# Kernel tuning notes

Hardware: AMD Instinct MI355X
Metric: run time of the kernel (lower is better)

## Reference

```python
import jax, jax.numpy as jnp
import numpy as np

D_MODEL = 1024
D_INDEX = 32
NUM_HEADS = 4
SEQ_LEN = 4096
BATCH = 2


def setup_inputs() -> dict:
    key = jax.random.key(0)
    ks = jax.random.split(key, 7)
    s = 1.0 / np.sqrt(D_MODEL)
    x = jax.random.normal(ks[0], (SEQ_LEN, BATCH, D_MODEL), dtype=jnp.float32)
    Wq = jax.random.uniform(ks[1], (D_MODEL, NUM_HEADS * D_INDEX), jnp.float32, -s, s)
    bq = jax.random.uniform(ks[2], (NUM_HEADS * D_INDEX,), jnp.float32, -s, s)
    Wk = jax.random.uniform(ks[3], (D_MODEL, D_INDEX), jnp.float32, -s, s)
    bk = jax.random.uniform(ks[4], (D_INDEX,), jnp.float32, -s, s)
    Ww = jax.random.uniform(ks[5], (D_MODEL, NUM_HEADS), jnp.float32, -s, s)
    bw = jax.random.uniform(ks[6], (NUM_HEADS,), jnp.float32, -s, s)
    return {"x": x, "Wq": Wq, "bq": bq, "Wk": Wk, "bk": bk, "Ww": Ww, "bw": bw}


def reference(x, Wq, bq, Wk, bk, Ww, bw):
    # x: [T, B, D] -> batch-first [B, T, D]
    xb = jnp.transpose(x, (1, 0, 2))
    B, T, _ = xb.shape
    q = (xb @ Wq + bq).reshape(B, T, NUM_HEADS, D_INDEX)  # [B,T,H,d]
    k = xb @ Wk + bk                                       # [B,T,d] (keys over s)
    w = xb @ Ww + bw                                       # [B,T,H]
    dot = jnp.einsum('bthd,bsd->btsh', q, k)               # [B,T,S,H]
    activated = jax.nn.relu(dot)
    # sum over heads weighted by w[b,t,h]
    index_scores = jnp.einsum('btsh,bth->bts', activated, w)
    return index_scores
```

## Files before the change

kernel.cpp:

```cpp
#include <hip/hip_runtime.h>

#define T_SEQ 4096
#define NBATCH 2
#define DM 1024
#define DI 32
#define NH 4
#define NCOLS 164
#define NCOLS_PAD 192
#define KC 64
#define BSTRIDE 72

typedef __attribute__((ext_vector_type(8))) short bf16x8;
typedef __attribute__((ext_vector_type(4))) float f32x4;

__device__ __forceinline__ unsigned short f2bf(float f) {
    unsigned int u = __builtin_bit_cast(unsigned int, f);
    u += 0x7FFFu + ((u >> 16) & 1u);
    return (unsigned short)(u >> 16);
}

__global__ __launch_bounds__(256) void prep_kernel(
    const float* __restrict__ Wq, const float* __restrict__ bq,
    const float* __restrict__ Wk, const float* __restrict__ bk,
    const float* __restrict__ Ww, const float* __restrict__ bw,
    unsigned short* __restrict__ WT, float* __restrict__ bias) {
    int c = blockIdx.x;
    const float* src = nullptr; int stride = 0; float bv = 0.f;
    if (c < 128)      { src = Wq + c;       stride = NH * DI; bv = bq[c]; }
    else if (c < 160) { src = Wk + (c-128); stride = DI;      bv = bk[c-128]; }
    else if (c < 164) { src = Ww + (c-160); stride = NH;      bv = bw[c-160]; }
    for (int k = threadIdx.x; k < DM; k += blockDim.x) {
        float v = src ? src[(size_t)k * stride] : 0.f;
        WT[(size_t)c * DM + k] = f2bf(v);
    }
    if (threadIdx.x == 0) bias[c] = bv;
}

__global__ __launch_bounds__(256) void proj_kernel(
    const float* __restrict__ x, const unsigned short* __restrict__ WT,
    const float* __restrict__ bias,
    unsigned short* __restrict__ qws, unsigned short* __restrict__ kws,
    float* __restrict__ wws) {
    __shared__ unsigned short Bb[2][NCOLS_PAD * BSTRIDE];
    __shared__ unsigned short Ab[2][1024];
    int t = threadIdx.x;
    int wave = t >> 6, lane = t & 63;
    int lr = lane & 15, kg = lane >> 4;
    int r0 = blockIdx.x * 16;

    int akk = t >> 7, alane = (t & 127) >> 1, ahalf = t & 1;
    int arow = alane & 15, akg = alane >> 4;
    int rowA = r0 + arow;
    int tA = rowA & (T_SEQ - 1), bA = rowA >> 12;
    const float* xrowA = x + ((size_t)tA * NBATCH + bA) * DM;

    bf16x8 breg[6];
    f32x4  areg;

    auto STAGE_LOAD = [&](int c) {
        int k0 = c * KC;
        #pragma unroll
        for (int it = 0; it < 6; ++it) {
            int tau = it * 256 + t;
            int col = tau >> 3, jg = tau & 7;
            breg[it] = *(const bf16x8*)(WT + (size_t)col * DM + k0 + jg * 8);
        }
        areg = *(const f32x4*)(xrowA + k0 + akk * 32 + akg * 8 + ahalf * 4);
    };
    auto STAGE_WRITE = [&](int buf) {
        #pragma unroll
        for (int it = 0; it < 6; ++it) {
            int tau = it * 256 + t;
            int col = tau >> 3, jg = tau & 7;
            *(bf16x8*)(&Bb[buf][col * BSTRIDE + jg * 8]) = breg[it];
        }
        unsigned short* d = &Ab[buf][akk * 512 + alane * 8 + ahalf * 4];
        d[0] = f2bf(areg[0]); d[1] = f2bf(areg[1]);
        d[2] = f2bf(areg[2]); d[3] = f2bf(areg[3]);
    };

    STAGE_LOAD(0);
    STAGE_WRITE(0);
    __syncthreads();

    int ct0 = wave * 3;
    f32x4 acc[3] = {};
    for (int c = 0; c < 16; ++c) {
        int buf = c & 1;
        if (c < 15) STAGE_LOAD(c + 1);
        #pragma unroll
        for (int kk = 0; kk < 2; ++kk) {
            bf16x8 af = *(const bf16x8*)(&Ab[buf][kk * 512 + lane * 8]);
            #pragma unroll
            for (int i = 0; i < 3; ++i) {
                int col = (ct0 + i) * 16 + lr;
                bf16x8 bfg = *(const bf16x8*)(&Bb[buf][col * BSTRIDE + kk * 32 + kg * 8]);
                acc[i] = __builtin_amdgcn_mfma_f32_16x16x32_bf16(af, bfg, acc[i], 0, 0, 0);
            }
        }
        if (c < 15) STAGE_WRITE(buf ^ 1);
        __syncthreads();
    }

    #pragma unroll
    for (int i = 0; i < 3; ++i) {
        int cout = (ct0 + i) * 16 + lr;
        float bv = bias[cout];
        #pragma unroll
        for (int r = 0; r < 4; ++r) {
            int rr = r0 + kg * 4 + r;
            int tt = rr & (T_SEQ - 1), bb = rr >> 12;
            float v = acc[i][r] + bv;
            size_t rowoff = (size_t)bb * T_SEQ + tt;
            if (cout < 128)       qws[rowoff * 128 + cout] = f2bf(v);
            else if (cout < 160)  kws[rowoff * 32 + (cout - 128)] = f2bf(v);
            else if (cout < 164)  wws[rowoff * 4 + (cout - 160)] = v;
        }
    }
}

__global__ __launch_bounds__(256) void indexer_kernel(
    const unsigned short* __restrict__ qws, const unsigned short* __restrict__ kws,
    const float* __restrict__ wws, float* __restrict__ out) {
    int wave = threadIdx.x >> 6;
    int lane = threadIdx.x & 63;
    int gw = blockIdx.x * 4 + wave;
    int strip = gw & 15;
    int t16 = (gw >> 4) & 255;
    int b = gw >> 12;
    int t0 = t16 * 16;
    int lr = lane & 15, kg = lane >> 4;

    const unsigned short* qrow = qws + ((size_t)b * T_SEQ + t0 + lr) * 128;
    bf16x8 qf[4];
    #pragma unroll
    for (int h = 0; h < 4; ++h)
        qf[h] = *(const bf16x8*)(qrow + h * 32 + kg * 8);

    f32x4 w4 = *(const f32x4*)(wws + ((size_t)b * T_SEQ + t0 + lr) * 4);

    float* outrow = out + (size_t)b * T_SEQ * T_SEQ + (size_t)(t0 + lr) * T_SEQ;
    const unsigned short* kbase = kws + (size_t)b * T_SEQ * 32;
    int sbase = strip * 256;

    for (int g = 0; g < 4; ++g) {
        int s0 = sbase + g * 64;
        bf16x8 kf0 = *(const bf16x8*)(kbase + (size_t)(s0      + lr) * 32 + kg * 8);
        bf16x8 kf1 = *(const bf16x8*)(kbase + (size_t)(s0 + 16 + lr) * 32 + kg * 8);
        bf16x8 kf2 = *(const bf16x8*)(kbase + (size_t)(s0 + 32 + lr) * 32 + kg * 8);
        bf16x8 kf3 = *(const bf16x8*)(kbase + (size_t)(s0 + 48 + lr) * 32 + kg * 8);
        f32x4 z = {0.f, 0.f, 0.f, 0.f};
        f32x4 v[4];
        #pragma unroll
        for (int j = 0; j < 4; ++j) {
            bf16x8 kf = (j == 0) ? kf0 : (j == 1) ? kf1 : (j == 2) ? kf2 : kf3;
            f32x4 a0 = __builtin_amdgcn_mfma_f32_16x16x32_bf16(kf, qf[0], z, 0, 0, 0);
            f32x4 a1 = __builtin_amdgcn_mfma_f32_16x16x32_bf16(kf, qf[1], z, 0, 0, 0);
            f32x4 a2 = __builtin_amdgcn_mfma_f32_16x16x32_bf16(kf, qf[2], z, 0, 0, 0);
            f32x4 a3 = __builtin_amdgcn_mfma_f32_16x16x32_bf16(kf, qf[3], z, 0, 0, 0);
            #pragma unroll
            for (int r = 0; r < 4; ++r) {
                v[j][r] = fmaxf(a0[r], 0.f) * w4[0] + fmaxf(a1[r], 0.f) * w4[1]
                        + fmaxf(a2[r], 0.f) * w4[2] + fmaxf(a3[r], 0.f) * w4[3];
            }
        }
        #pragma unroll
        for (int j = 0; j < 4; ++j)
            *(f32x4*)(outrow + s0 + j * 16 + kg * 4) = v[j];
    }
}

extern "C" void kernel_launch(void* const* d_in, const int* in_sizes, int n_in,
                              void* d_out, int out_size, void* d_ws, size_t ws_size,
                              hipStream_t stream) {
    const float* x  = (const float*)d_in[0];
    const float* Wq = (const float*)d_in[1];
    const float* bq = (const float*)d_in[2];
    const float* Wk = (const float*)d_in[3];
    const float* bk = (const float*)d_in[4];
    const float* Ww = (const float*)d_in[5];
    const float* bw = (const float*)d_in[6];
    float* out = (float*)d_out;

    char* ws = (char*)d_ws;
    unsigned short* WT  = (unsigned short*)(ws);
    float* bias         = (float*)(ws + 393216);
    unsigned short* qws = (unsigned short*)(ws + 524288);
    unsigned short* kws = (unsigned short*)(ws + 2621440);
    float* wws          = (float*)(ws + 3145728);

    prep_kernel<<<dim3(NCOLS_PAD), dim3(256), 0, stream>>>(Wq, bq, Wk, bk, Ww, bw, WT, bias);
    proj_kernel<<<dim3(512), dim3(256), 0, stream>>>(x, WT, bias, qws, kws, wws);
    indexer_kernel<<<dim3(2048), dim3(256), 0, stream>>>(qws, kws, wws, out);
}
```

Baseline: 58.06 us.

## Stage indexer output tiles through LDS for fully coalesced row stores

The indexer kernel now assigns a block to 16 query rows and a 1024-wide key range. Each wave writes its MFMA results into a double-buffered shared-memory tile, then the block writes full 1 KB contiguous row segments to global memory. Previously each lane stored 16-byte pieces scattered across 16 different output rows. This targets store coalescing on the 128 MB output write, at the cost of LDS traffic and a barrier per iteration.

```diff
diff --git a/kernel.cpp b/kernel.cpp
--- a/kernel.cpp
+++ b/kernel.cpp
@@ -9,6 +9,7 @@
 #define NCOLS_PAD 192
 #define KC 64
 #define BSTRIDE 72
+#define SROW 264
 
 typedef __attribute__((ext_vector_type(8))) short bf16x8;
 typedef __attribute__((ext_vector_type(4))) float f32x4;
@@ -53,6 +54,7 @@
     int rowA = r0 + arow;
     int tA = rowA & (T_SEQ - 1), bA = rowA >> 12;
     const float* xrowA = x + ((size_t)tA * NBATCH + bA) * DM;
+    (void)akg;
 
     bf16x8 breg[6];
     f32x4  areg;
@@ -65,7 +67,7 @@
             int col = tau >> 3, jg = tau & 7;
             breg[it] = *(const bf16x8*)(WT + (size_t)col * DM + k0 + jg * 8);
         }
-        areg = *(const f32x4*)(xrowA + k0 + akk * 32 + akg * 8 + ahalf * 4);
+        areg = *(const f32x4*)(xrowA + k0 + akk * 32 + (alane >> 4) * 8 + ahalf * 4);
     };
     auto STAGE_WRITE = [&](int buf) {
         #pragma unroll
@@ -122,14 +124,18 @@
 __global__ __launch_bounds__(256) void indexer_kernel(
     const unsigned short* __restrict__ qws, const unsigned short* __restrict__ kws,
     const float* __restrict__ wws, float* __restrict__ out) {
-    int wave = threadIdx.x >> 6;
-    int lane = threadIdx.x & 63;
-    int gw = blockIdx.x * 4 + wave;
-    int strip = gw & 15;
-    int t16 = (gw >> 4) & 255;
-    int b = gw >> 12;
+    __shared__ float sbuf[2][16 * SROW];
+    int t = threadIdx.x;
+    int wave = t >> 6;
+    int lane = t & 63;
+    int lr = lane & 15, kg = lane >> 4;
+
+    int blk = blockIdx.x;
+    int b = blk >> 10;
+    int rem = blk & 1023;
+    int t16 = rem >> 2;
+    int sblk = rem & 3;
     int t0 = t16 * 16;
-    int lr = lane & 15, kg = lane >> 4;
 
     const unsigned short* qrow = qws + ((size_t)b * T_SEQ + t0 + lr) * 128;
     bf16x8 qf[4];
@@ -139,12 +145,12 @@
 
     f32x4 w4 = *(const f32x4*)(wws + ((size_t)b * T_SEQ + t0 + lr) * 4);
 
-    float* outrow = out + (size_t)b * T_SEQ * T_SEQ + (size_t)(t0 + lr) * T_SEQ;
     const unsigned short* kbase = kws + (size_t)b * T_SEQ * 32;
-    int sbase = strip * 256;
+    float* outb = out + (size_t)b * T_SEQ * T_SEQ;
+    int tl = t & 63, ws = t >> 6;
 
     for (int g = 0; g < 4; ++g) {
-        int s0 = sbase + g * 64;
+        int s0 = sblk * 1024 + g * 256 + wave * 64;
         bf16x8 kf0 = *(const bf16x8*)(kbase + (size_t)(s0      + lr) * 32 + kg * 8);
         bf16x8 kf1 = *(const bf16x8*)(kbase + (size_t)(s0 + 16 + lr) * 32 + kg * 8);
         bf16x8 kf2 = *(const bf16x8*)(kbase + (size_t)(s0 + 32 + lr) * 32 + kg * 8);
@@ -164,9 +170,19 @@
                         + fmaxf(a2[r], 0.f) * w4[2] + fmaxf(a3[r], 0.f) * w4[3];
             }
         }
+        float* dst = &sbuf[g & 1][lr * SROW + wave * 64 + kg * 4];
         #pragma unroll
         for (int j = 0; j < 4; ++j)
-            *(f32x4*)(outrow + s0 + j * 16 + kg * 4) = v[j];
+            *(f32x4*)(dst + j * 16) = v[j];
+        __syncthreads();
+        const float* srcb = &sbuf[g & 1][0];
+        size_t colbase = (size_t)sblk * 1024 + g * 256;
+        #pragma unroll
+        for (int i = 0; i < 4; ++i) {
+            int row16 = i * 4 + ws;
+            f32x4 val = *(const f32x4*)(srcb + row16 * SROW + tl * 4);
+            *(f32x4*)(outb + (size_t)(t0 + row16) * T_SEQ + colbase + tl * 4) = val;
+        }
     }
 }
 
```

Measured after the change: 60.78 us. 1.05x slower.

## Double proj rows per block and pre-tile weights for contiguous chunk loads

Applied to the files above, without the earlier changes.

The projection kernel now processes 32 rows per block with 512 threads, so each staged weight chunk in shared memory is reused by twice as many rows and total weight traffic from global memory is halved. The prep kernel writes the bf16 weights in a K-chunk-major tiled layout, so each chunk load is one contiguous stream. The trade-off is half as many blocks (256) on a large GPU, which lowers parallelism and occupancy for this stage, plus larger blocks.

```diff
diff --git a/kernel.cpp b/kernel.cpp
--- a/kernel.cpp
+++ b/kernel.cpp
@@ -23,7 +23,7 @@
     const float* __restrict__ Wq, const float* __restrict__ bq,
     const float* __restrict__ Wk, const float* __restrict__ bk,
     const float* __restrict__ Ww, const float* __restrict__ bw,
-    unsigned short* __restrict__ WT, float* __restrict__ bias) {
+    unsigned short* __restrict__ WT2, float* __restrict__ bias) {
     int c = blockIdx.x;
     const float* src = nullptr; int stride = 0; float bv = 0.f;
     if (c < 128)      { src = Wq + c;       stride = NH * DI; bv = bq[c]; }
@@ -31,50 +31,50 @@
     else if (c < 164) { src = Ww + (c-160); stride = NH;      bv = bw[c-160]; }
     for (int k = threadIdx.x; k < DM; k += blockDim.x) {
         float v = src ? src[(size_t)k * stride] : 0.f;
-        WT[(size_t)c * DM + k] = f2bf(v);
+        WT2[((size_t)(k >> 6) * NCOLS_PAD + c) * KC + (k & 63)] = f2bf(v);
     }
     if (threadIdx.x == 0) bias[c] = bv;
 }
 
-__global__ __launch_bounds__(256) void proj_kernel(
-    const float* __restrict__ x, const unsigned short* __restrict__ WT,
+__global__ __launch_bounds__(512) void proj_kernel(
+    const float* __restrict__ x, const unsigned short* __restrict__ WT2,
     const float* __restrict__ bias,
     unsigned short* __restrict__ qws, unsigned short* __restrict__ kws,
     float* __restrict__ wws) {
     __shared__ unsigned short Bb[2][NCOLS_PAD * BSTRIDE];
-    __shared__ unsigned short Ab[2][1024];
+    __shared__ unsigned short Ab[2][2048];
     int t = threadIdx.x;
     int wave = t >> 6, lane = t & 63;
     int lr = lane & 15, kg = lane >> 4;
-    int r0 = blockIdx.x * 16;
+    int r0 = blockIdx.x * 32;
 
-    int akk = t >> 7, alane = (t & 127) >> 1, ahalf = t & 1;
-    int arow = alane & 15, akg = alane >> 4;
-    int rowA = r0 + arow;
-    int tA = rowA & (T_SEQ - 1), bA = rowA >> 12;
+    int ahalf = t & 1, alane = (t >> 1) & 63, akk = (t >> 7) & 1, arh = t >> 8;
+    int arow = r0 + arh * 16 + (alane & 15);
+    int tA = arow & (T_SEQ - 1), bA = arow >> 12;
     const float* xrowA = x + ((size_t)tA * NBATCH + bA) * DM;
+    int aoff = akk * 32 + (alane >> 4) * 8 + ahalf * 4;
+    int adst = arh * 1024 + akk * 512 + alane * 8 + ahalf * 4;
 
-    bf16x8 breg[6];
+    bf16x8 breg[3];
     f32x4  areg;
 
     auto STAGE_LOAD = [&](int c) {
-        int k0 = c * KC;
+        const unsigned short* wp = WT2 + (size_t)c * (NCOLS_PAD * KC);
         #pragma unroll
-        for (int it = 0; it < 6; ++it) {
-            int tau = it * 256 + t;
-            int col = tau >> 3, jg = tau & 7;
-            breg[it] = *(const bf16x8*)(WT + (size_t)col * DM + k0 + jg * 8);
+        for (int it = 0; it < 3; ++it) {
+            int tau = it * 512 + t;
+            breg[it] = *(const bf16x8*)(wp + tau * 8);
         }
-        areg = *(const f32x4*)(xrowA + k0 + akk * 32 + akg * 8 + ahalf * 4);
+        areg = *(const f32x4*)(xrowA + c * KC + aoff);
     };
     auto STAGE_WRITE = [&](int buf) {
         #pragma unroll
-        for (int it = 0; it < 6; ++it) {
-            int tau = it * 256 + t;
+        for (int it = 0; it < 3; ++it) {
+            int tau = it * 512 + t;
             int col = tau >> 3, jg = tau & 7;
             *(bf16x8*)(&Bb[buf][col * BSTRIDE + jg * 8]) = breg[it];
         }
-        unsigned short* d = &Ab[buf][akk * 512 + alane * 8 + ahalf * 4];
+        unsigned short* d = &Ab[buf][adst];
         d[0] = f2bf(areg[0]); d[1] = f2bf(areg[1]);
         d[2] = f2bf(areg[2]); d[3] = f2bf(areg[3]);
     };
@@ -83,14 +83,15 @@
     STAGE_WRITE(0);
     __syncthreads();
 
-    int ct0 = wave * 3;
+    int ct0 = (wave >> 1) * 3;
+    int rh  = wave & 1;
     f32x4 acc[3] = {};
     for (int c = 0; c < 16; ++c) {
         int buf = c & 1;
         if (c < 15) STAGE_LOAD(c + 1);
         #pragma unroll
         for (int kk = 0; kk < 2; ++kk) {
-            bf16x8 af = *(const bf16x8*)(&Ab[buf][kk * 512 + lane * 8]);
+            bf16x8 af = *(const bf16x8*)(&Ab[buf][rh * 1024 + kk * 512 + lane * 8]);
             #pragma unroll
             for (int i = 0; i < 3; ++i) {
                 int col = (ct0 + i) * 16 + lr;
@@ -108,7 +109,7 @@
         float bv = bias[cout];
         #pragma unroll
         for (int r = 0; r < 4; ++r) {
-            int rr = r0 + kg * 4 + r;
+            int rr = r0 + rh * 16 + kg * 4 + r;
             int tt = rr & (T_SEQ - 1), bb = rr >> 12;
             float v = acc[i][r] + bv;
             size_t rowoff = (size_t)bb * T_SEQ + tt;
@@ -183,13 +184,13 @@
     float* out = (float*)d_out;
 
     char* ws = (char*)d_ws;
-    unsigned short* WT  = (unsigned short*)(ws);
+    unsigned short* WT2 = (unsigned short*)(ws);
     float* bias         = (float*)(ws + 393216);
     unsigned short* qws = (unsigned short*)(ws + 524288);
     unsigned short* kws = (unsigned short*)(ws + 2621440);
     float* wws          = (float*)(ws + 3145728);
 
-    prep_kernel<<<dim3(NCOLS_PAD), dim3(256), 0, stream>>>(Wq, bq, Wk, bk, Ww, bw, WT, bias);
-    proj_kernel<<<dim3(512), dim3(256), 0, stream>>>(x, WT, bias, qws, kws, wws);
+    prep_kernel<<<dim3(NCOLS_PAD), dim3(256), 0, stream>>>(Wq, bq, Wk, bk, Ww, bw, WT2, bias);
+    proj_kernel<<<dim3(256), dim3(512), 0, stream>>>(x, WT2, bias, qws, kws, wws);
     indexer_kernel<<<dim3(2048), dim3(256), 0, stream>>>(qws, kws, wws, out);
 }
```

New measurement: 58.98 us. Within noise of the previous version (+1.6%).
